# Optimization experiments

Measured on AMD Instinct MI355X. Metric: run time of the kernel, lower is better.

## Reference

```python
import jax, jax.numpy as jnp
import numpy as np

N_CLUSTERS = 131072
N_CENTROIDS = 256
D_FEAT = 64
N_BATCH = 8
COORD_RANGE = 128


def setup_inputs() -> dict:
    key = jax.random.key(0)
    k1, k2, k3, k4, k5, k6 = jax.random.split(key, 6)
    # coords: column 0 = batch index, columns 1:4 = integer xyz voxel coords
    clu_batch = jax.random.randint(k1, (N_CLUSTERS, 1), 0, N_BATCH, dtype=jnp.int32)
    clu_xyz = jax.random.randint(k2, (N_CLUSTERS, 3), 0, COORD_RANGE, dtype=jnp.int32)
    cluster_coords = jnp.concatenate([clu_batch, clu_xyz], axis=1)
    # guarantee every batch has >= 1 centroid (avoids empty-softmax rows)
    cen_batch = (jnp.arange(N_CENTROIDS, dtype=jnp.int32) % N_BATCH)[:, None]
    cen_xyz = jax.random.randint(k3, (N_CENTROIDS, 3), 0, COORD_RANGE, dtype=jnp.int32)
    centroid_coords = jnp.concatenate([cen_batch, cen_xyz], axis=1)
    cluster_feats = jax.random.normal(k4, (N_CLUSTERS, D_FEAT), dtype=jnp.float32)
    centroid_feats = jax.random.normal(k5, (N_CENTROIDS, D_FEAT), dtype=jnp.float32)
    return {
        "cluster_coords": cluster_coords,
        "cluster_feats": cluster_feats,
        "centroid_coords": centroid_coords,
        "centroid_feats": centroid_feats,
    }


def reference(cluster_coords, cluster_feats, centroid_coords, centroid_feats):
    # Per-batch pairwise-distance softmax attention, matmul, scatter into dense
    # [N, M] output filled with -inf for cross-batch pairs. Vectorized form of
    # the original python loop over batch indices: since each (cluster, centroid)
    # pair is touched only when batches match, a batch-equality mask + masked
    # softmax reproduces the per-batch math exactly.
    same_batch = cluster_coords[:, 0][:, None] == centroid_coords[:, 0][None, :]  # [N, M]

    # distances from integer xyz coords (no_grad in original -> stop_gradient, and
    # coords are ints anyway)
    diff = (cluster_coords[:, None, 1:] - centroid_coords[None, :, 1:]).astype(cluster_feats.dtype)  # [N, M, 3]
    dists = jnp.maximum(jnp.sqrt(jnp.sum(diff * diff, axis=-1)), 0.1)  # clamp(min=0.1)
    logits = jnp.where(same_batch, -dists, -jnp.inf)
    attn = jax.lax.stop_gradient(jax.nn.softmax(logits, axis=-1))  # [N, M], per-batch softmax

    scores = jnp.clip(cluster_feats @ centroid_feats.T * attn, -10.0, 10.0)  # [N, M]
    out = jnp.where(same_batch, scores, -jnp.inf)
    return out
```

## Files before the change

### kernel.cpp

```cpp
#include <hip/hip_runtime.h>
#include <hip/hip_fp16.h>

constexpr int N_CLUSTERS   = 131072;
constexpr int N_CENTROIDS  = 256;
constexpr int D_FEAT       = 64;

constexpr int THREADS        = 512;
constexpr int ROWS_PER_BLOCK = 128;

#define MASK_VAL (-1.0e30f)

typedef __attribute__((ext_vector_type(8))) short bf16x8;
typedef __attribute__((ext_vector_type(4))) float f32x4;
typedef __attribute__((ext_vector_type(2))) __fp16 h2;

static __device__ inline unsigned pk2t(float a, float b) {
    return __builtin_amdgcn_perm(__float_as_uint(b), __float_as_uint(a), 0x07060302u);
}
static __device__ inline unsigned pk4h(float a, float b, float c, float d) {
    h2 p01 = __builtin_amdgcn_cvt_pkrtz(a, b);
    h2 p23 = __builtin_amdgcn_cvt_pkrtz(c, d);
    unsigned lo, hi;
    __builtin_memcpy(&lo, &p01, 4);
    __builtin_memcpy(&hi, &p23, 4);
    return __builtin_amdgcn_perm(hi, lo, 0x05040100u);
}
static __device__ inline float h2f_lo(unsigned u) {
    return __half2float(__ushort_as_half((unsigned short)(u & 0xFFFFu)));
}
static __device__ inline float h2f_hi(unsigned u) {
    return __half2float(__ushort_as_half((unsigned short)(u >> 16)));
}

__global__ __launch_bounds__(THREADS, 8)
void instance_head_kernel(const int*   __restrict__ clu_coords,
                          const float* __restrict__ clu_feats,
                          const int*   __restrict__ cen_coords,
                          const float* __restrict__ cen_feats,
                          float*       __restrict__ out)
{
    __shared__ unsigned Bl[16 * 2 * 64 * 4];
    __shared__ float4   pccf[N_CENTROIDS];

    const int t    = threadIdx.x;
    const int lane = t & 63;
    const int wave = __builtin_amdgcn_readfirstlane(t >> 6);
    const int m    = lane & 15;
    const int quad = lane >> 4;
    const int r0w  = blockIdx.x * ROWS_PER_BLOCK + wave * 16;

    const float* bptr = clu_feats + (size_t)(r0w + m) * D_FEAT + quad * 8;
    const float4 bL0 = *(const float4*)(bptr);
    const float4 bH0 = *(const float4*)(bptr + 4);
    const float4 bL1 = *(const float4*)(bptr + 32);
    const float4 bH1 = *(const float4*)(bptr + 36);

    #pragma unroll
    for (int i = 0; i < 4; ++i) {
        const int q = t + i * THREADS;
        const int n = q >> 3, o = q & 7;
        const float4 g0 = ((const float4*)cen_feats)[q * 2];
        const float4 g1 = ((const float4*)cen_feats)[q * 2 + 1];
        uint4 d;
        d.x = pk2t(g0.x, g0.y); d.y = pk2t(g0.z, g0.w);
        d.z = pk2t(g1.x, g1.y); d.w = pk2t(g1.z, g1.w);
        const int tile = n >> 4;
        const int np   = n & 15;
        const int f    = o >> 2;
        const int lp   = (np | ((o & 3) << 4)) ^ o;
        ((uint4*)Bl)[(tile * 2 + f) * 64 + lp] = d;
    }
    if (t < N_CENTROIDS) {
        const int4 c = ((const int4*)cen_coords)[t];
        pccf[t] = make_float4((float)c.x, (float)c.y, (float)c.z, (float)c.w);
    }

    const int4  rc = ((const int4*)clu_coords)[r0w + m];
    const float fb = (float)rc.x;
    const float fx = (float)rc.y, fy = (float)rc.z, fz = (float)rc.w;

    union { uint4 u; bf16x8 v; } b0, b1;
    b0.u.x = pk2t(bL0.x, bL0.y); b0.u.y = pk2t(bL0.z, bL0.w);
    b0.u.z = pk2t(bH0.x, bH0.y); b0.u.w = pk2t(bH0.z, bH0.w);
    b1.u.x = pk2t(bL1.x, bL1.y); b1.u.y = pk2t(bL1.z, bL1.w);
    b1.u.z = pk2t(bH1.x, bH1.y); b1.u.w = pk2t(bH1.z, bH1.w);

    __syncthreads();

    unsigned u16[16];
    float rsum = 0.f;
    #pragma unroll
    for (int tt = 0; tt < 16; ++tt) {
        float uu[4];
        #pragma unroll
        for (int i = 0; i < 4; ++i) {
            const float4 cf = pccf[tt * 16 + quad * 4 + i];
            const float dx = fx - cf.y, dy = fy - cf.z, dz = fz - cf.w;
            const float d2   = fmaf(dx, dx, fmaf(dy, dy, dz * dz));
            const float dist = fmaxf(__builtin_sqrtf(d2), 0.1f);
            const float e    = __expf(-dist);
            const bool  same = (fb == cf.x);
            rsum += same ? e : 0.f;
            uu[i] = same ? e : -1.0f;
        }
        u16[tt] = pk4h(uu[0], uu[1], uu[2], uu[3]);
    }
    rsum += __shfl_xor(rsum, 16, 64);
    rsum += __shfl_xor(rsum, 32, 64);
    const float inv = (rsum > 1e-37f) ? __builtin_amdgcn_rcpf(rsum) : 0.f;

    const int sl0 = lane ^ quad;
    const int sl1 = sl0 ^ 4;
    float* obase = out + (size_t)(r0w + m) * N_CENTROIDS + quad * 4;

    #pragma unroll
    for (int tt = 0; tt < 16; ++tt) {
        const bf16x8 aC0 = *(const bf16x8*)&Bl[((tt * 2 + 0) * 64 + sl0) * 4];
        const bf16x8 aC1 = *(const bf16x8*)&Bl[((tt * 2 + 1) * 64 + sl1) * 4];
        f32x4 acc = {0.f, 0.f, 0.f, 0.f};
        acc = __builtin_amdgcn_mfma_f32_16x16x32_bf16(aC0, b0.v, acc, 0, 0, 0);
        acc = __builtin_amdgcn_mfma_f32_16x16x32_bf16(aC1, b1.v, acc, 0, 0, 0);

        const unsigned up = u16[tt];
        const unsigned uq = u16[tt] >> 16;
        float uu[4];
        uu[0] = h2f_lo(up); uu[1] = h2f_hi(up);
        uu[2] = h2f_lo(uq); uu[3] = h2f_hi(uq);
        float4 o;
        #pragma unroll
        for (int i = 0; i < 4; ++i) {
            float w = acc[i] * (fmaxf(uu[i], 0.f) * inv);
            w = fminf(fmaxf(w, -10.f), 10.f);
            (&o.x)[i] = (uu[i] < 0.f) ? MASK_VAL : w;
        }
        *(float4*)(obase + tt * 16) = o;
    }
}

extern "C" void kernel_launch(void* const* d_in, const int* in_sizes, int n_in,
                              void* d_out, int out_size, void* d_ws, size_t ws_size,
                              hipStream_t stream) {
    const int*   clu_coords = (const int*)  d_in[0];
    const float* clu_feats  = (const float*)d_in[1];
    const int*   cen_coords = (const int*)  d_in[2];
    const float* cen_feats  = (const float*)d_in[3];
    float* out = (float*)d_out;

    dim3 grid(N_CLUSTERS / ROWS_PER_BLOCK);
    dim3 block(THREADS);
    instance_head_kernel<<<grid, block, 0, stream>>>(
        clu_coords, clu_feats, cen_coords, cen_feats, out);
}
```

Measured before the change: 171.6 us.

## Compute squared distances and batch mask via bf16 MFMA expansion

Rewrites the per-pair squared distance as an expanded dot product, |p|^2 - 2p·c + |c|^2, plus a large penalty term 131072*(pb-pc)^2 that encodes batch mismatch. The dot product is evaluated with a bf16 MFMA, and norms are split into hi/lo bf16 parts to keep precision. This replaces the per-element LDS coordinate loads and the FMA distance math, and the batch-equality test becomes a threshold on d2. In exchange it relies on bf16 exactness for small integer coordinates and on the penalty overflowing so the exp of masked pairs is zero, which is fragile numerically.

```diff
diff --git a/kernel.cpp b/kernel.cpp
--- a/kernel.cpp
+++ b/kernel.cpp
@@ -9,6 +9,7 @@
 constexpr int ROWS_PER_BLOCK = 128;
 
 #define MASK_VAL (-1.0e30f)
+#define TH_MASK  (65536.0f)
 
 typedef __attribute__((ext_vector_type(8))) short bf16x8;
 typedef __attribute__((ext_vector_type(4))) float f32x4;
@@ -40,7 +41,7 @@
                           float*       __restrict__ out)
 {
     __shared__ unsigned Bl[16 * 2 * 64 * 4];
-    __shared__ float4   pccf[N_CENTROIDS];
+    __shared__ uint4    Atab[N_CENTROIDS];
 
     const int t    = threadIdx.x;
     const int lane = t & 63;
@@ -72,12 +73,37 @@
     }
     if (t < N_CENTROIDS) {
         const int4 c = ((const int4*)cen_coords)[t];
-        pccf[t] = make_float4((float)c.x, (float)c.y, (float)c.z, (float)c.w);
+        const float gx = (float)c.y, gy = (float)c.z, gz = (float)c.w, gb = (float)c.x;
+        const float cn = fmaf(gx, gx, fmaf(gy, gy, gz * gz));
+        const float hi = __uint_as_float(__float_as_uint(cn) & 0xFFFF0000u);
+        const float lo = cn - hi;
+        uint4 e;
+        e.x = pk2t(-2.f * gx, -2.f * gy);
+        e.y = pk2t(-2.f * gz, -262144.f * gb);
+        e.z = pk2t(hi, lo);
+        e.w = pk2t(131072.f * gb * gb, 1.0f);
+        Atab[t] = e;
     }
 
-    const int4  rc = ((const int4*)clu_coords)[r0w + m];
-    const float fb = (float)rc.x;
-    const float fx = (float)rc.y, fy = (float)rc.z, fz = (float)rc.w;
+    const int4 rc = ((const int4*)clu_coords)[r0w + m];
+    union { uint4 u; bf16x8 v; } bc;
+    {
+        const float px = (float)rc.y, py = (float)rc.z, pz = (float)rc.w, pb = (float)rc.x;
+        const float pn  = fmaf(px, px, fmaf(py, py, pz * pz));
+        const float phi = __uint_as_float(__float_as_uint(pn) & 0xFFFF0000u);
+        const float plo = pn - phi;
+        uint4 q0, q1, zz;
+        q0.x = pk2t(px, py);
+        q0.y = pk2t(pz, pb);
+        q0.z = 0x3F803F80u;
+        q0.w = pk2t(1.0f, phi);
+        q1.x = pk2t(plo, 131072.f * pb * pb);
+        q1.y = 0u; q1.z = 0u; q1.w = 0u;
+        zz.x = 0u; zz.y = 0u; zz.z = 0u; zz.w = 0u;
+        bc.u = (quad == 0) ? q0 : ((quad == 1) ? q1 : zz);
+    }
+    const unsigned amsk = (quad == 0) ? 0xFFFFFFFFu : 0u;
+    const unsigned aor  = (quad == 1) ? 0x3F803F80u : 0u;
 
     union { uint4 u; bf16x8 v; } b0, b1;
     b0.u.x = pk2t(bL0.x, bL0.y); b0.u.y = pk2t(bL0.z, bL0.w);
@@ -91,17 +117,21 @@
     float rsum = 0.f;
     #pragma unroll
     for (int tt = 0; tt < 16; ++tt) {
+        const uint4 a = Atab[tt * 16 + m];
+        union { uint4 u; bf16x8 v; } af;
+        af.u.x = (a.x & amsk) | aor;
+        af.u.y =  a.y & amsk;
+        af.u.z =  a.z & amsk;
+        af.u.w =  a.w & amsk;
+        f32x4 d2 = {0.f, 0.f, 0.f, 0.f};
+        d2 = __builtin_amdgcn_mfma_f32_16x16x32_bf16(af.v, bc.v, d2, 0, 0, 0);
         float uu[4];
         #pragma unroll
         for (int i = 0; i < 4; ++i) {
-            const float4 cf = pccf[tt * 16 + quad * 4 + i];
-            const float dx = fx - cf.y, dy = fy - cf.z, dz = fz - cf.w;
-            const float d2   = fmaf(dx, dx, fmaf(dy, dy, dz * dz));
-            const float dist = fmaxf(__builtin_sqrtf(d2), 0.1f);
+            const float dist = fmaxf(__builtin_sqrtf(d2[i]), 0.1f);
             const float e    = __expf(-dist);
-            const bool  same = (fb == cf.x);
-            rsum += same ? e : 0.f;
-            uu[i] = same ? e : -1.0f;
+            rsum += e;
+            uu[i] = (d2[i] < TH_MASK) ? e : -1.0f;
         }
         u16[tt] = pk4h(uu[0], uu[1], uu[2], uu[3]);
     }
```

Result: slower. 175.2 us (+2.1%).
